# Performance work log

Hardware: AMD Instinct MI355X
Metric: run time of the kernel (lower is better)

## Reference

```python
import math
import jax, jax.numpy as jnp
import numpy as np

B, T, D, L, E = 2, 1024, 1024, 12, 4
EPS = 1e-5


def _ln(v, g, b):
    mu = jnp.mean(v, axis=-1, keepdims=True)
    var = jnp.mean(jnp.square(v - mu), axis=-1, keepdims=True)
    return (v - mu) * jax.lax.rsqrt(var + EPS) * g + b


def setup_inputs() -> dict:
    key = jax.random.key(0)
    ks = jax.random.split(key, 4)
    x = jax.random.normal(ks[0], (B, T, D), dtype=jnp.float32)
    queries = jax.random.normal(ks[1], (L, D), dtype=jnp.float32) * 0.02
    W1 = jax.random.normal(ks[2], (L, D, E * D), dtype=jnp.float32) * 0.02
    W2 = jax.random.normal(ks[3], (L, E * D, D), dtype=jnp.float32) * 0.02
    return {
        'x': x,
        'queries': queries,
        'kn_g': jnp.ones((L, D), jnp.float32),
        'kn_b': jnp.zeros((L, D), jnp.float32),
        'ln_g': jnp.ones((L, D), jnp.float32),
        'ln_b': jnp.zeros((L, D), jnp.float32),
        'W1': W1,
        'b1': jnp.zeros((L, E * D), jnp.float32),
        'W2': W2,
        'b2': jnp.zeros((L, D), jnp.float32),
    }


def reference(x, queries, kn_g, kn_b, ln_g, ln_b, W1, b1, W2, b2):
    scale = 1.0 / math.sqrt(D)
    history = [x]
    h = x
    for l in range(L):
        V = jnp.stack(history, axis=0)              # (l+1, B, T, D)
        K = _ln(V, kn_g[l], kn_b[l])
        scores = jnp.einsum('d,lbtd->lbt', queries[l], K) * scale
        alpha = jax.nn.softmax(scores, axis=0)       # softmax over history axis
        residual = jnp.einsum('lbt,lbtd->btd', alpha, V)
        u = _ln(h, ln_g[l], ln_b[l])
        ff = jax.nn.gelu(u @ W1[l] + b1[l], approximate=False) @ W2[l] + b2[l]
        h = residual + ff
        history.append(h)
    return h
```

## Files before the change

kernel.cpp:

```cpp
#include <hip/hip_runtime.h>
#include <math.h>

#define BATCH 2
#define TSEQ 1024
#define DIM 1024
#define NLAYER 12
#define EDIM 4096
#define BT 2048
#define EPS_LN 1e-5f
#define NZ2 4

typedef __attribute__((ext_vector_type(4))) float  f32x4;
typedef __attribute__((ext_vector_type(8))) __bf16 bf16x8;
typedef __attribute__((ext_vector_type(4))) __bf16 bf16x4;

__device__ __forceinline__ void gl_lds16(const void* gptr, void* lptr) {
    __builtin_amdgcn_global_load_lds(
        (const __attribute__((address_space(1))) void*)gptr,
        (__attribute__((address_space(3))) void*)lptr,
        16, 0, 0);
}

__device__ __forceinline__ void wtile256(float (*t)[65], const float* src,
                                         __bf16* dst, int R, int C,
                                         int rt, int ct, int tid)
{
    int lr = tid >> 2, cs = (tid & 3) << 4;
    const float* sp = src + (size_t)(rt * 64 + lr) * C + ct * 64 + cs;
#pragma unroll
    for (int s = 0; s < 4; s++) {
        f32x4 v = *(const f32x4*)(sp + s * 4);
        t[lr][cs + s * 4 + 0] = v[0];
        t[lr][cs + s * 4 + 1] = v[1];
        t[lr][cs + s * 4 + 2] = v[2];
        t[lr][cs + s * 4 + 3] = v[3];
    }
    __syncthreads();
    int oc = tid >> 2, rs = (tid & 3) << 4;
    bf16x8 o0, o1;
#pragma unroll
    for (int e = 0; e < 8; e++) o0[e] = (__bf16)t[rs + e][oc];
#pragma unroll
    for (int e = 0; e < 8; e++) o1[e] = (__bf16)t[rs + 8 + e][oc];
    __bf16* dp = dst + (size_t)(ct * 64 + oc) * R + rt * 64 + rs;
    *(bf16x8*)dp = o0;
    *(bf16x8*)(dp + 8) = o1;
}

__global__ __launch_bounds__(256) void wtrans_kernel(
    const float* __restrict__ W1, const float* __restrict__ W2,
    __bf16* __restrict__ W1t, __bf16* __restrict__ W2t)
{
    __shared__ float t[64][65];
    int z = blockIdx.z;
    if (z == 0) wtile256(t, W1, W1t, DIM, EDIM, blockIdx.y, blockIdx.x, threadIdx.x);
    else        wtile256(t, W2, W2t, EDIM, DIM, blockIdx.x, blockIdx.y, threadIdx.x);
}

__global__ __launch_bounds__(256)
void attn_wt_kernel(const float* __restrict__ x,
                    const __bf16* __restrict__ baseprev,
                    __bf16* __restrict__ histbf,
                    const __bf16* __restrict__ part,
                    const float* __restrict__ q,
                    const float* __restrict__ kng,
                    const float* __restrict__ knb,
                    const float* __restrict__ lng,
                    const float* __restrict__ lnb,
                    const float* __restrict__ b2,
                    __bf16* __restrict__ hnext,
                    __bf16* __restrict__ u,
                    int nl,
                    const float* __restrict__ W1n,
                    const float* __restrict__ W2n,
                    __bf16* __restrict__ W1tn,
                    __bf16* __restrict__ W2tn,
                    int dowt)
{
    __shared__ char smem[49408];

    if (blockIdx.x >= BT) {
        if (!dowt) return;
        float (*t)[65] = (float(*)[65])smem;
        int tile = blockIdx.x - BT;
        if (tile < 1024) wtile256(t, W1n, W1tn, DIM, EDIM, tile >> 6, tile & 63, threadIdx.x);
        else { int t3 = tile - 1024; wtile256(t, W2n, W2tn, EDIM, DIM, t3 & 63, t3 >> 6, threadIdx.x); }
        return;
    }

    float (*V)[DIM] = (float(*)[DIM])smem;
    float* sS  = (float*)(smem + 49152);
    float* sMu = sS + NLAYER;
    float* sRs = sMu + NLAYER;

    const int bt = blockIdx.x;
    const int tid = threadIdx.x, lane = tid & 63, w = tid >> 6;

    f32x4 gqv[4];
    float sg = 0.f, sb = 0.f;
#pragma unroll
    for (int i = 0; i < 4; i++) {
        int d = i * 256 + lane * 4;
        f32x4 g4 = *(const f32x4*)(kng + d);
        f32x4 q4 = *(const f32x4*)(q + d);
        f32x4 b4 = *(const f32x4*)(knb + d);
#pragma unroll
        for (int c = 0; c < 4; c++) {
            float gq = g4[c] * q4[c];
            gqv[i][c] = gq;
            sg += gq;
            sb += b4[c] * q4[c];
        }
    }
#pragma unroll
    for (int off = 32; off; off >>= 1) {
        sg += __shfl_xor(sg, off);
        sb += __shfl_xor(sb, off);
    }

    for (int lp = w; lp < nl; lp += 4) {
        f32x4 vv[4];
        if (lp == nl - 1) {
            if (nl == 1) {
                const float* vp = x + (size_t)bt * DIM;
#pragma unroll
                for (int i = 0; i < 4; i++) vv[i] = *(const f32x4*)(vp + i * 256 + lane * 4);
            } else {
                const __bf16* vp = baseprev + (size_t)bt * DIM;
#pragma unroll
                for (int i = 0; i < 4; i++) {
                    bf16x4 b4 = *(const bf16x4*)(vp + i * 256 + lane * 4);
#pragma unroll
                    for (int c = 0; c < 4; c++) vv[i][c] = (float)b4[c];
                }
            }
            if (part) {
#pragma unroll
                for (int z = 0; z < NZ2; z++) {
                    const __bf16* pp = part + ((size_t)z * BT + bt) * DIM;
#pragma unroll
                    for (int i = 0; i < 4; i++) {
                        bf16x4 p4 = *(const bf16x4*)(pp + i * 256 + lane * 4);
#pragma unroll
                        for (int c = 0; c < 4; c++) vv[i][c] += (float)p4[c];
                    }
                }
            }
            if (nl < NLAYER) {
                __bf16* mp = histbf + ((size_t)lp * BT + bt) * DIM;
#pragma unroll
                for (int i = 0; i < 4; i++) {
                    bf16x4 m4;
#pragma unroll
                    for (int c = 0; c < 4; c++) m4[c] = (__bf16)vv[i][c];
                    *(bf16x4*)(mp + i * 256 + lane * 4) = m4;
                }
            }
        } else {
            const __bf16* mp = histbf + ((size_t)lp * BT + bt) * DIM;
#pragma unroll
            for (int i = 0; i < 4; i++) {
                bf16x4 m4 = *(const bf16x4*)(mp + i * 256 + lane * 4);
#pragma unroll
                for (int c = 0; c < 4; c++) vv[i][c] = (float)m4[c];
            }
        }

        float s1 = 0.f, s2 = 0.f, sq = 0.f;
#pragma unroll
        for (int i = 0; i < 4; i++) {
            *(f32x4*)(&V[lp][i * 256 + lane * 4]) = vv[i];
#pragma unroll
            for (int c = 0; c < 4; c++) {
                float xv = vv[i][c];
                s1 += xv; s2 += xv * xv; sq += xv * gqv[i][c];
            }
        }
#pragma unroll
        for (int off = 32; off; off >>= 1) {
            s1 += __shfl_xor(s1, off);
            s2 += __shfl_xor(s2, off);
            sq += __shfl_xor(sq, off);
        }
        if (lane == 0) {
            float mu = s1 * (1.0f / DIM);
            float var = s2 * (1.0f / DIM) - mu * mu;
            float rs = rsqrtf(var + EPS_LN);
            sMu[lp] = mu; sRs[lp] = rs;
            sS[lp] = (rs * (sq - mu * sg) + sb) * (1.0f / 32.0f);
        }
    }
    __syncthreads();

    float mx = -1e30f;
#pragma unroll
    for (int i = 0; i < NLAYER; i++) if (i < nl) mx = fmaxf(mx, sS[i]);
    float al[NLAYER];
    float ssum = 0.f;
#pragma unroll
    for (int i = 0; i < NLAYER; i++) {
        al[i] = (i < nl) ? __expf(sS[i] - mx) : 0.f;
        ssum += al[i];
    }
    float inv = 1.0f / ssum;

    const int d = tid * 4;
    f32x4 r; r[0] = 0.f; r[1] = 0.f; r[2] = 0.f; r[3] = 0.f;
#pragma unroll
    for (int i = 0; i < NLAYER; i++) {
        if (i < nl) {
            f32x4 v4 = *(const f32x4*)(&V[i][d]);
            float a = al[i] * inv;
            r[0] += a * v4[0]; r[1] += a * v4[1]; r[2] += a * v4[2]; r[3] += a * v4[3];
        }
    }
    f32x4 h4 = *(const f32x4*)(&V[nl - 1][d]);
    f32x4 b24 = *(const f32x4*)(b2 + d);
    bf16x4 ho;
#pragma unroll
    for (int c = 0; c < 4; c++) ho[c] = (__bf16)(r[c] + b24[c]);
    *(bf16x4*)(hnext + (size_t)bt * DIM + d) = ho;

    float mu = sMu[nl - 1], rs = sRs[nl - 1];
    f32x4 g4 = *(const f32x4*)(lng + d);
    f32x4 b4 = *(const f32x4*)(lnb + d);
    bf16x4 uo;
#pragma unroll
    for (int c = 0; c < 4; c++) uo[c] = (__bf16)((h4[c] - mu) * rs * g4[c] + b4[c]);
    *(bf16x4*)(u + (size_t)bt * DIM + d) = uo;
}

#define STG 49152

template <int EPI>
__global__ __launch_bounds__(512, 1)
void gemm8(const __bf16* __restrict__ A, const __bf16* __restrict__ Bt,
           const float* __restrict__ bias, void* __restrict__ outp,
           int N, int As, int Bs)
{
    __shared__ char lds[3 * STG];
    const int tid = threadIdx.x, lane = tid & 63, w = tid >> 6;
    const int wm = w >> 2, wn = w & 3;
    const int lr = lane & 15;
    const int hib = (lane >> 4) << 4;
    const int NT = 16;

    const int fid = blockIdx.x;
    const int xcd = fid & 7;
    const int c = fid >> 3;
    int m0, n0, kbase, zsl;
    if (EPI == 0) {
        int mi = ((xcd & 1) << 3) + (c & 7);
        int ni = ((xcd >> 1) << 2) + (c >> 3);
        m0 = mi * 128; n0 = ni * 256; kbase = 0; zsl = 0;
    } else {
        zsl = c & 3;
        int local = c >> 2;
        int mi = ((xcd & 3) << 2) + (local & 3);
        int ni = ((xcd >> 2) << 1) + (local >> 2);
        m0 = mi * 128; n0 = ni * 256; kbase = zsl * 1024;
    }

    f32x4 acc[4][4];
#pragma unroll
    for (int i = 0; i < 4; i++)
#pragma unroll
        for (int j2 = 0; j2 < 4; j2++) { acc[i][j2][0]=0.f; acc[i][j2][1]=0.f; acc[i][j2][2]=0.f; acc[i][j2][3]=0.f; }

    const int srow = tid >> 3;
    const int ksrc = ((tid & 7) << 4) ^ ((srow & 7) << 4);
    const char* Ac = (const char*)A;
    const char* Bc = (const char*)Bt;
    size_t aoff[2], boff[4];
#pragma unroll
    for (int cc = 0; cc < 2; cc++)
        aoff[cc] = ((size_t)(m0 + cc * 64 + srow) * As + kbase) * 2 + ksrc;
#pragma unroll
    for (int cc = 0; cc < 4; cc++)
        boff[cc] = ((size_t)(n0 + cc * 64 + srow) * Bs + kbase) * 2 + ksrc;

    char* abw = lds + w * 1024;
    char* bbw = lds + 16384 + w * 1024;

    auto STAGE = [&](int tt, int bi) {
        size_t kb = (size_t)tt * 128;
        char* ab = abw + bi * STG;
        char* bb = bbw + bi * STG;
#pragma unroll
        for (int cc = 0; cc < 2; cc++) gl_lds16(Ac + aoff[cc] + kb, ab + cc * 8192);
#pragma unroll
        for (int cc = 0; cc < 4; cc++) gl_lds16(Bc + boff[cc] + kb, bb + cc * 8192);
    };

    STAGE(0, 0);
    STAGE(1, 1);

    int sb = 0, st = 2;
#pragma unroll 1
    for (int t = 0; t < NT; ++t) {
        if (t < NT - 1) asm volatile("s_waitcnt vmcnt(6)" ::: "memory");
        else            asm volatile("s_waitcnt vmcnt(0)" ::: "memory");
        __builtin_amdgcn_s_barrier();
        __builtin_amdgcn_sched_barrier(0);

        if (t + 2 < NT) STAGE(t + 2, st);

        const char* base = lds + sb * STG;
        bf16x8 af[2][4], bfr[2][4];
#pragma unroll
        for (int kk = 0; kk < 2; kk++) {
#pragma unroll
            for (int i = 0; i < 4; i++) {
                int ra = wm * 64 + i * 16 + lr;
                af[kk][i] = *(const bf16x8*)(base + ra * 128 + ((kk * 64 + hib) ^ ((ra & 7) << 4)));
            }
#pragma unroll
            for (int j2 = 0; j2 < 4; j2++) {
                int rb = wn * 64 + j2 * 16 + lr;
                bfr[kk][j2] = *(const bf16x8*)(base + 16384 + rb * 128 + ((kk * 64 + hib) ^ ((rb & 7) << 4)));
            }
        }
        __builtin_amdgcn_s_setprio(1);
#pragma unroll
        for (int kk = 0; kk < 2; kk++)
#pragma unroll
            for (int i = 0; i < 4; i++)
#pragma unroll
                for (int j2 = 0; j2 < 4; j2++)
                    acc[i][j2] = __builtin_amdgcn_mfma_f32_16x16x32_bf16(af[kk][i], bfr[kk][j2], acc[i][j2], 0, 0, 0);
        __builtin_amdgcn_s_setprio(0);

        sb = (sb == 2) ? 0 : sb + 1;
        st = (st == 2) ? 0 : st + 1;
    }

    const int lrow = (lane >> 4) << 2;
    if (EPI == 0) {
        __bf16* out = (__bf16*)outp;
#pragma unroll
        for (int i = 0; i < 4; i++) {
#pragma unroll
            for (int j2 = 0; j2 < 4; j2++) {
                int colg = n0 + wn * 64 + j2 * 16 + lr;
                float bc = bias[colg];
#pragma unroll
                for (int r = 0; r < 4; r++) {
                    int rowg = m0 + wm * 64 + i * 16 + lrow + r;
                    float v = acc[i][j2][r] + bc;
                    float tt2 = 0.7978845608f * (v + 0.044715f * v * v * v);
                    float e = __expf(2.0f * tt2);
                    float th = 1.0f - 2.0f / (e + 1.0f);
                    out[(size_t)rowg * N + colg] = (__bf16)(0.5f * v * (1.0f + th));
                }
            }
        }
    } else {
        __bf16* out = (__bf16*)outp + (size_t)zsl * BT * N;
#pragma unroll
        for (int i = 0; i < 4; i++) {
#pragma unroll
            for (int j2 = 0; j2 < 4; j2++) {
                int colg = n0 + wn * 64 + j2 * 16 + lr;
#pragma unroll
                for (int r = 0; r < 4; r++) {
                    int rowg = m0 + wm * 64 + i * 16 + lrow + r;
                    out[(size_t)rowg * N + colg] = (__bf16)acc[i][j2][r];
                }
            }
        }
    }
}

__global__ void final_reduce(const __bf16* __restrict__ base,
                             const __bf16* __restrict__ part,
                             float* __restrict__ out)
{
    size_t i = ((size_t)blockIdx.x * 256 + threadIdx.x) * 4;
    bf16x4 b4 = *(const bf16x4*)(base + i);
    f32x4 r;
#pragma unroll
    for (int c = 0; c < 4; c++) r[c] = (float)b4[c];
#pragma unroll
    for (int z = 0; z < NZ2; z++) {
        bf16x4 p = *(const bf16x4*)(part + (size_t)z * BT * DIM + i);
#pragma unroll
        for (int c = 0; c < 4; c++) r[c] += (float)p[c];
    }
    *(f32x4*)(out + i) = r;
}

extern "C" void kernel_launch(void* const* d_in, const int* in_sizes, int n_in,
                              void* d_out, int out_size, void* d_ws, size_t ws_size,
                              hipStream_t stream)
{
    const float* x   = (const float*)d_in[0];
    const float* q   = (const float*)d_in[1];
    const float* kng = (const float*)d_in[2];
    const float* knb = (const float*)d_in[3];
    const float* lng = (const float*)d_in[4];
    const float* lnb = (const float*)d_in[5];
    const float* W1  = (const float*)d_in[6];
    const float* b1  = (const float*)d_in[7];
    const float* W2  = (const float*)d_in[8];
    const float* b2  = (const float*)d_in[9];

    char* ws = (char*)d_ws;
    const size_t MB = 1048576;
    __bf16* base2[2] = { (__bf16*)(ws), (__bf16*)(ws + 4 * MB) };
    __bf16* histbf = (__bf16*)(ws + 8 * MB);
    __bf16* ubuf   = (__bf16*)(ws + 56 * MB);
    __bf16* hmid   = (__bf16*)(ws + 60 * MB);
    __bf16* W1tb[2] = { (__bf16*)(ws + 76 * MB), (__bf16*)(ws + 84 * MB) };
    __bf16* W2tb[2] = { (__bf16*)(ws + 92 * MB), (__bf16*)(ws + 100 * MB) };
    __bf16* part   = (__bf16*)(ws + 108 * MB);

    wtrans_kernel<<<dim3(64, 16, 2), 256, 0, stream>>>(W1, W2, W1tb[0], W2tb[0]);

    for (int l = 0; l < NLAYER; l++) {
        int nl = l + 1;
        int ln = (l + 1 < NLAYER) ? l + 1 : l;
        __bf16* hnext = base2[l & 1];
        const __bf16* bprev = base2[(l + 1) & 1];
        attn_wt_kernel<<<dim3(2 * BT), 256, 0, stream>>>(
            x, bprev, histbf, (l >= 1) ? part : (const __bf16*)nullptr,
            q + (size_t)l * DIM,
            kng + (size_t)l * DIM, knb + (size_t)l * DIM,
            lng + (size_t)l * DIM, lnb + (size_t)l * DIM,
            b2 + (size_t)l * DIM, hnext, ubuf, nl,
            W1 + (size_t)ln * DIM * EDIM, W2 + (size_t)ln * EDIM * DIM,
            W1tb[(l + 1) & 1], W2tb[(l + 1) & 1], (l + 1 < NLAYER) ? 1 : 0);
        gemm8<0><<<dim3(256), 512, 0, stream>>>(
            ubuf, W1tb[l & 1], b1 + (size_t)l * EDIM, (void*)hmid, EDIM, DIM, DIM);
        gemm8<2><<<dim3(256), 512, 0, stream>>>(
            hmid, W2tb[l & 1], nullptr, (void*)part, DIM, EDIM, EDIM);
    }

    final_reduce<<<dim3(BT * DIM / 1024), 256, 0, stream>>>(
        base2[1], part, (float*)d_out);
}
```

Before: 866.1 us.

## Swap GEMM operands to compute transposed tiles and stage epilogue through LDS

The FFN GEMMs now take the transposed weights as the A operand and activations as B, so each block computes an output tile with weight-output rows and activation columns. The result is transposed back through LDS with an XOR swizzle and written as 16-byte vector stores instead of scattered 2-byte stores. The block-to-tile mapping is simplified, dropping the XCD-aware swizzle. The change targets uncoalesced epilogue stores, at the cost of extra LDS traffic and barriers and possibly worse L2 locality from the simpler tile mapping.

```diff
diff --git a/kernel.cpp b/kernel.cpp
--- a/kernel.cpp
+++ b/kernel.cpp
@@ -234,32 +234,24 @@
 
 template <int EPI>
 __global__ __launch_bounds__(512, 1)
-void gemm8(const __bf16* __restrict__ A, const __bf16* __restrict__ Bt,
+void gemmT(const __bf16* __restrict__ A, const __bf16* __restrict__ Bt,
            const float* __restrict__ bias, void* __restrict__ outp,
-           int N, int As, int Bs)
+           int As, int Bs)
 {
     __shared__ char lds[3 * STG];
     const int tid = threadIdx.x, lane = tid & 63, w = tid >> 6;
     const int wm = w >> 2, wn = w & 3;
     const int lr = lane & 15;
-    const int hib = (lane >> 4) << 4;
+    const int hi = lane >> 4;
+    const int hib = hi << 4;
     const int NT = 16;
 
     const int fid = blockIdx.x;
-    const int xcd = fid & 7;
+    const int ni = fid & 7;
     const int c = fid >> 3;
     int m0, n0, kbase, zsl;
-    if (EPI == 0) {
-        int mi = ((xcd & 1) << 3) + (c & 7);
-        int ni = ((xcd >> 1) << 2) + (c >> 3);
-        m0 = mi * 128; n0 = ni * 256; kbase = 0; zsl = 0;
-    } else {
-        zsl = c & 3;
-        int local = c >> 2;
-        int mi = ((xcd & 3) << 2) + (local & 3);
-        int ni = ((xcd >> 2) << 1) + (local >> 2);
-        m0 = mi * 128; n0 = ni * 256; kbase = zsl * 1024;
-    }
+    if (EPI == 0) { m0 = c * 128; n0 = ni * 256; kbase = 0; zsl = 0; }
+    else { zsl = c & 3; m0 = (c >> 2) * 128; n0 = ni * 256; kbase = zsl * 1024; }
 
     f32x4 acc[4][4];
 #pragma unroll
@@ -334,39 +326,48 @@
         st = (st == 2) ? 0 : st + 1;
     }
 
-    const int lrow = (lane >> 4) << 2;
-    if (EPI == 0) {
-        __bf16* out = (__bf16*)outp;
+    __syncthreads();
+    {
+        char* eb = lds;
 #pragma unroll
         for (int i = 0; i < 4; i++) {
+            int mb = wm * 64 + i * 16 + hi * 4;
+            float bc[4];
+            if (EPI == 0) {
+#pragma unroll
+                for (int r = 0; r < 4; r++) bc[r] = bias[m0 + mb + r];
+            }
 #pragma unroll
             for (int j2 = 0; j2 < 4; j2++) {
-                int colg = n0 + wn * 64 + j2 * 16 + lr;
-                float bc = bias[colg];
+                int nn = wn * 64 + j2 * 16 + lr;
+                bf16x4 v;
 #pragma unroll
                 for (int r = 0; r < 4; r++) {
-                    int rowg = m0 + wm * 64 + i * 16 + lrow + r;
-                    float v = acc[i][j2][r] + bc;
-                    float tt2 = 0.7978845608f * (v + 0.044715f * v * v * v);
-                    float e = __expf(2.0f * tt2);
-                    float th = 1.0f - 2.0f / (e + 1.0f);
-                    out[(size_t)rowg * N + colg] = (__bf16)(0.5f * v * (1.0f + th));
+                    float vv = acc[i][j2][r];
+                    if (EPI == 0) {
+                        vv += bc[r];
+                        float tt2 = 0.7978845608f * (vv + 0.044715f * vv * vv * vv);
+                        float e = __expf(2.0f * tt2);
+                        float th = 1.0f - 2.0f / (e + 1.0f);
+                        vv = 0.5f * vv * (1.0f + th);
+                    }
+                    v[r] = (__bf16)vv;
                 }
-            }
-        }
-    } else {
-        __bf16* out = (__bf16*)outp + (size_t)zsl * BT * N;
-#pragma unroll
-        for (int i = 0; i < 4; i++) {
-#pragma unroll
-            for (int j2 = 0; j2 < 4; j2++) {
-                int colg = n0 + wn * 64 + j2 * 16 + lr;
-#pragma unroll
-                for (int r = 0; r < 4; r++) {
-                    int rowg = m0 + wm * 64 + i * 16 + lrow + r;
-                    out[(size_t)rowg * N + colg] = (__bf16)acc[i][j2][r];
-                }
-            }
+                *(bf16x4*)(eb + nn * 256 + ((mb * 2) ^ ((nn & 7) << 4))) = v;
+            }
+        }
+        __syncthreads();
+
+        const int row = tid >> 1, half = tid & 1;
+        const int RS = (EPI == 0) ? EDIM : DIM;
+        __bf16* ob = (EPI == 0) ? (__bf16*)outp
+                                : (__bf16*)outp + (size_t)zsl * BT * DIM;
+        char* gout = (char*)(ob + (size_t)(n0 + row) * RS + m0 + half * 64);
+        const char* src = eb + row * 256;
+#pragma unroll
+        for (int c8 = 0; c8 < 8; c8++) {
+            uint4 v = *(const uint4*)(src + (((half * 128) + c8 * 16) ^ ((row & 7) << 4)));
+            *(uint4*)(gout + c8 * 16) = v;
         }
     }
 }
@@ -429,10 +430,10 @@
             b2 + (size_t)l * DIM, hnext, ubuf, nl,
             W1 + (size_t)ln * DIM * EDIM, W2 + (size_t)ln * EDIM * DIM,
             W1tb[(l + 1) & 1], W2tb[(l + 1) & 1], (l + 1 < NLAYER) ? 1 : 0);
-        gemm8<0><<<dim3(256), 512, 0, stream>>>(
-            ubuf, W1tb[l & 1], b1 + (size_t)l * EDIM, (void*)hmid, EDIM, DIM, DIM);
-        gemm8<2><<<dim3(256), 512, 0, stream>>>(
-            hmid, W2tb[l & 1], nullptr, (void*)part, DIM, EDIM, EDIM);
+        gemmT<0><<<dim3(256), 512, 0, stream>>>(
+            W1tb[l & 1], ubuf, b1 + (size_t)l * EDIM, (void*)hmid, DIM, DIM);
+        gemmT<2><<<dim3(256), 512, 0, stream>>>(
+            W2tb[l & 1], hmid, nullptr, (void*)part, EDIM, EDIM);
     }
 
     final_reduce<<<dim3(BT * DIM / 1024), 256, 0, stream>>>(
```

After: 984.7 us. 1.14x slower.

## Switch GEMMs to 256x256 tiles with K=32 steps and 4-stage pipeline

Applied to the files above, without the earlier changes.

Replaces the 128x256 tile GEMM (K-step 64, 3-stage LDS ring, 256 blocks) with a 256x256 tile GEMM that uses K-step 32, a 4-slot LDS ring and 128 blocks. This raises arithmetic intensity per block and deepens the prefetch pipeline, and it drops the XCD-aware block mapping. The cost is that only 128 blocks run on a 256-CU part, so half the CUs sit idle. It also doubles the accumulator registers per thread, which may pressure occupancy.

```diff
diff --git a/kernel.cpp b/kernel.cpp
--- a/kernel.cpp
+++ b/kernel.cpp
@@ -230,123 +230,108 @@
     *(bf16x4*)(u + (size_t)bt * DIM + d) = uo;
 }
 
-#define STG 49152
+#define NU 32
 
 template <int EPI>
 __global__ __launch_bounds__(512, 1)
-void gemm8(const __bf16* __restrict__ A, const __bf16* __restrict__ Bt,
-           const float* __restrict__ bias, void* __restrict__ outp,
-           int N, int As, int Bs)
-{
-    __shared__ char lds[3 * STG];
+void gemm256k32(const __bf16* __restrict__ A, const __bf16* __restrict__ Bt,
+                const float* __restrict__ bias, void* __restrict__ outp,
+                int N, int As, int Bs)
+{
+    __shared__ char lds[131072];
     const int tid = threadIdx.x, lane = tid & 63, w = tid >> 6;
     const int wm = w >> 2, wn = w & 3;
     const int lr = lane & 15;
     const int hib = (lane >> 4) << 4;
-    const int NT = 16;
 
     const int fid = blockIdx.x;
-    const int xcd = fid & 7;
-    const int c = fid >> 3;
     int m0, n0, kbase, zsl;
     if (EPI == 0) {
-        int mi = ((xcd & 1) << 3) + (c & 7);
-        int ni = ((xcd >> 1) << 2) + (c >> 3);
-        m0 = mi * 128; n0 = ni * 256; kbase = 0; zsl = 0;
+        m0 = (fid >> 4) * 256; n0 = (fid & 15) * 256; kbase = 0; zsl = 0;
     } else {
-        zsl = c & 3;
-        int local = c >> 2;
-        int mi = ((xcd & 3) << 2) + (local & 3);
-        int ni = ((xcd >> 2) << 1) + (local >> 2);
-        m0 = mi * 128; n0 = ni * 256; kbase = zsl * 1024;
-    }
-
-    f32x4 acc[4][4];
-#pragma unroll
-    for (int i = 0; i < 4; i++)
-#pragma unroll
-        for (int j2 = 0; j2 < 4; j2++) { acc[i][j2][0]=0.f; acc[i][j2][1]=0.f; acc[i][j2][2]=0.f; acc[i][j2][3]=0.f; }
-
-    const int srow = tid >> 3;
-    const int ksrc = ((tid & 7) << 4) ^ ((srow & 7) << 4);
+        zsl = fid & 3;
+        m0 = ((fid >> 2) & 7) * 256; n0 = (fid >> 5) * 256; kbase = zsl * 1024;
+    }
+
+    f32x4 acc[8][4];
+#pragma unroll
+    for (int i = 0; i < 8; i++)
+#pragma unroll
+        for (int j = 0; j < 4; j++) { acc[i][j][0]=0.f; acc[i][j][1]=0.f; acc[i][j][2]=0.f; acc[i][j][3]=0.f; }
+
     const char* Ac = (const char*)A;
     const char* Bc = (const char*)Bt;
-    size_t aoff[2], boff[4];
-#pragma unroll
-    for (int cc = 0; cc < 2; cc++)
-        aoff[cc] = ((size_t)(m0 + cc * 64 + srow) * As + kbase) * 2 + ksrc;
-#pragma unroll
-    for (int cc = 0; cc < 4; cc++)
-        boff[cc] = ((size_t)(n0 + cc * 64 + srow) * Bs + kbase) * 2 + ksrc;
-
-    char* abw = lds + w * 1024;
-    char* bbw = lds + 16384 + w * 1024;
-
-    auto STAGE = [&](int tt, int bi) {
-        size_t kb = (size_t)tt * 128;
-        char* ab = abw + bi * STG;
-        char* bb = bbw + bi * STG;
-#pragma unroll
-        for (int cc = 0; cc < 2; cc++) gl_lds16(Ac + aoff[cc] + kb, ab + cc * 8192);
-#pragma unroll
-        for (int cc = 0; cc < 4; cc++) gl_lds16(Bc + boff[cc] + kb, bb + cc * 8192);
+    size_t ag[2], bg[2];
+    int ldso[2];
+#pragma unroll
+    for (int l = 0; l < 2; l++) {
+        int idx = l * 512 + tid;
+        int row = idx >> 2, qq = idx & 3;
+        int ksw = (qq * 16) ^ ((row & 3) << 4);
+        ag[l] = ((size_t)(m0 + row) * As + kbase) * 2 + ksw;
+        bg[l] = ((size_t)(n0 + row) * Bs + kbase) * 2 + ksw;
+        ldso[l] = l * 8192 + w * 1024;
+    }
+
+    auto STAGE = [&](int uu, int slot) {
+        size_t kb = (size_t)uu * 64;
+        char* sa = lds + slot * 32768;
+        char* sbp = sa + 16384;
+#pragma unroll
+        for (int l = 0; l < 2; l++) gl_lds16(Ac + ag[l] + kb, sa + ldso[l]);
+#pragma unroll
+        for (int l = 0; l < 2; l++) gl_lds16(Bc + bg[l] + kb, sbp + ldso[l]);
     };
 
     STAGE(0, 0);
     STAGE(1, 1);
-
-    int sb = 0, st = 2;
+    STAGE(2, 2);
+
 #pragma unroll 1
-    for (int t = 0; t < NT; ++t) {
-        if (t < NT - 1) asm volatile("s_waitcnt vmcnt(6)" ::: "memory");
-        else            asm volatile("s_waitcnt vmcnt(0)" ::: "memory");
+    for (int u = 0; u < NU; ++u) {
+        if (u < NU - 2)       asm volatile("s_waitcnt vmcnt(8)" ::: "memory");
+        else if (u == NU - 2) asm volatile("s_waitcnt vmcnt(4)" ::: "memory");
+        else                  asm volatile("s_waitcnt vmcnt(0)" ::: "memory");
         __builtin_amdgcn_s_barrier();
         __builtin_amdgcn_sched_barrier(0);
 
-        if (t + 2 < NT) STAGE(t + 2, st);
-
-        const char* base = lds + sb * STG;
-        bf16x8 af[2][4], bfr[2][4];
-#pragma unroll
-        for (int kk = 0; kk < 2; kk++) {
-#pragma unroll
-            for (int i = 0; i < 4; i++) {
-                int ra = wm * 64 + i * 16 + lr;
-                af[kk][i] = *(const bf16x8*)(base + ra * 128 + ((kk * 64 + hib) ^ ((ra & 7) << 4)));
-            }
-#pragma unroll
-            for (int j2 = 0; j2 < 4; j2++) {
-                int rb = wn * 64 + j2 * 16 + lr;
-                bfr[kk][j2] = *(const bf16x8*)(base + 16384 + rb * 128 + ((kk * 64 + hib) ^ ((rb & 7) << 4)));
-            }
+        if (u + 3 < NU) STAGE(u + 3, (u + 3) & 3);
+
+        const char* sa = lds + (u & 3) * 32768;
+        const char* sbp = sa + 16384;
+        bf16x8 bfr[4], afr[8];
+#pragma unroll
+        for (int j = 0; j < 4; j++) {
+            int row = wn * 64 + j * 16 + lr;
+            bfr[j] = *(const bf16x8*)(sbp + row * 64 + (hib ^ ((row & 3) << 4)));
+        }
+#pragma unroll
+        for (int i = 0; i < 8; i++) {
+            int row = wm * 128 + i * 16 + lr;
+            afr[i] = *(const bf16x8*)(sa + row * 64 + (hib ^ ((row & 3) << 4)));
         }
         __builtin_amdgcn_s_setprio(1);
 #pragma unroll
-        for (int kk = 0; kk < 2; kk++)
-#pragma unroll
-            for (int i = 0; i < 4; i++)
-#pragma unroll
-                for (int j2 = 0; j2 < 4; j2++)
-                    acc[i][j2] = __builtin_amdgcn_mfma_f32_16x16x32_bf16(af[kk][i], bfr[kk][j2], acc[i][j2], 0, 0, 0);
+        for (int i = 0; i < 8; i++)
+#pragma unroll
+            for (int j = 0; j < 4; j++)
+                acc[i][j] = __builtin_amdgcn_mfma_f32_16x16x32_bf16(afr[i], bfr[j], acc[i][j], 0, 0, 0);
         __builtin_amdgcn_s_setprio(0);
-
-        sb = (sb == 2) ? 0 : sb + 1;
-        st = (st == 2) ? 0 : st + 1;
     }
 
     const int lrow = (lane >> 4) << 2;
     if (EPI == 0) {
         __bf16* out = (__bf16*)outp;
 #pragma unroll
-        for (int i = 0; i < 4; i++) {
-#pragma unroll
-            for (int j2 = 0; j2 < 4; j2++) {
-                int colg = n0 + wn * 64 + j2 * 16 + lr;
+        for (int i = 0; i < 8; i++) {
+#pragma unroll
+            for (int j = 0; j < 4; j++) {
+                int colg = n0 + wn * 64 + j * 16 + lr;
                 float bc = bias[colg];
 #pragma unroll
                 for (int r = 0; r < 4; r++) {
-                    int rowg = m0 + wm * 64 + i * 16 + lrow + r;
-                    float v = acc[i][j2][r] + bc;
+                    int rowg = m0 + wm * 128 + i * 16 + lrow + r;
+                    float v = acc[i][j][r] + bc;
                     float tt2 = 0.7978845608f * (v + 0.044715f * v * v * v);
                     float e = __expf(2.0f * tt2);
                     float th = 1.0f - 2.0f / (e + 1.0f);
@@ -357,14 +342,14 @@
     } else {
         __bf16* out = (__bf16*)outp + (size_t)zsl * BT * N;
 #pragma unroll
-        for (int i = 0; i < 4; i++) {
-#pragma unroll
-            for (int j2 = 0; j2 < 4; j2++) {
-                int colg = n0 + wn * 64 + j2 * 16 + lr;
+        for (int i = 0; i < 8; i++) {
+#pragma unroll
+            for (int j = 0; j < 4; j++) {
+                int colg = n0 + wn * 64 + j * 16 + lr;
 #pragma unroll
                 for (int r = 0; r < 4; r++) {
-                    int rowg = m0 + wm * 64 + i * 16 + lrow + r;
-                    out[(size_t)rowg * N + colg] = (__bf16)acc[i][j2][r];
+                    int rowg = m0 + wm * 128 + i * 16 + lrow + r;
+                    out[(size_t)rowg * N + colg] = (__bf16)acc[i][j][r];
                 }
             }
         }
@@ -429,9 +414,9 @@
             b2 + (size_t)l * DIM, hnext, ubuf, nl,
             W1 + (size_t)ln * DIM * EDIM, W2 + (size_t)ln * EDIM * DIM,
             W1tb[(l + 1) & 1], W2tb[(l + 1) & 1], (l + 1 < NLAYER) ? 1 : 0);
-        gemm8<0><<<dim3(256), 512, 0, stream>>>(
+        gemm256k32<0><<<dim3(128), 512, 0, stream>>>(
             ubuf, W1tb[l & 1], b1 + (size_t)l * EDIM, (void*)hmid, EDIM, DIM, DIM);
-        gemm8<2><<<dim3(256), 512, 0, stream>>>(
+        gemm256k32<2><<<dim3(128), 512, 0, stream>>>(
             hmid, W2tb[l & 1], nullptr, (void*)part, DIM, EDIM, EDIM);
     }
 
```

After: 1.251 ms. 1.44x slower.
